# Performance work log

Hardware: AMD Instinct MI355X
Metric: run time of the kernel (lower is better)

Reference implementation:

```python
import jax, jax.numpy as jnp
import numpy as np

B, T, D, V, L = 32, 512, 512, 1024, 128
BLANK = 0
NEG = -1e30  # log-domain 'minus infinity' that is fp-safe


def setup_inputs() -> dict:
    key = jax.random.key(0)
    k1, k2, k3 = jax.random.split(key, 3)
    x = jax.random.normal(k1, (B, T, D), dtype=jnp.float32)
    W = jax.random.normal(k2, (D, V), dtype=jnp.float32) / np.sqrt(D).astype(np.float32)
    b = jnp.zeros((V,), dtype=jnp.float32)
    # CTC targets must be in [1, V) (never the blank id 0)
    target = jax.random.randint(k3, (B, L), 1, V)
    input_lengths = jnp.full((B,), T, dtype=jnp.int32)
    target_lengths = jnp.full((B,), L, dtype=jnp.int32)
    return {"x": x, "W": W, "b": b, "target": target,
            "input_lengths": input_lengths, "target_lengths": target_lengths}


def _ctc_loss(log_probs, target, input_lengths, target_lengths):
    # log_probs: [T, B, V] (time-major), target: [B, L]
    Tt, Bb, _ = log_probs.shape
    Ll = target.shape[1]
    S = 2 * Ll + 1  # extended label sequence: blank,t0,blank,t1,...,blank
    ext = jnp.full((Bb, S), BLANK, dtype=target.dtype).at[:, 1::2].set(target)  # [B,S]
    ext_m2 = jnp.pad(ext, ((0, 0), (2, 0)), constant_values=BLANK)[:, :S]
    skip = (ext != BLANK) & (ext != ext_m2) & (jnp.arange(S)[None, :] >= 2)  # [B,S]

    # gather log-probs of extended labels for every time step: [T,B,S]
    lp_ext = jnp.take_along_axis(log_probs, jnp.broadcast_to(ext[None], (Tt, Bb, S)), axis=2)

    alpha0 = jnp.full((Bb, S), NEG, log_probs.dtype)
    alpha0 = alpha0.at[:, 0].set(lp_ext[0, :, 0]).at[:, 1].set(lp_ext[0, :, 1])

    def step(alpha, lp_t):
        a1 = jnp.pad(alpha, ((0, 0), (1, 0)), constant_values=NEG)[:, :S]
        a2 = jnp.pad(alpha, ((0, 0), (2, 0)), constant_values=NEG)[:, :S]
        c = jnp.logaddexp(alpha, a1)
        c = jnp.where(skip, jnp.logaddexp(c, a2), c)
        new = c + lp_t
        return new, new

    _, alphas = jax.lax.scan(step, alpha0, lp_ext[1:])
    alphas = jnp.concatenate([alpha0[None], alphas], axis=0)  # [T,B,S]

    bi = jnp.arange(Bb)
    a_last = alphas[input_lengths - 1, bi]  # [B,S] alpha at each sample's final frame
    ll = jnp.logaddexp(a_last[bi, 2 * target_lengths - 1], a_last[bi, 2 * target_lengths])
    nll = -ll  # per-sample negative log-likelihood
    # zero_infinity=True: infinite losses are zeroed
    nll = jnp.where(jnp.isinf(nll) | (nll > 1e29), 0.0, nll)
    # reduction='mean': divide each loss by its target length, then mean
    return jnp.mean(nll / jnp.maximum(target_lengths, 1).astype(nll.dtype))


def reference(x, W, b, target, input_lengths, target_lengths):
    logits = jnp.einsum('btd,dv->btv', x, W) + b  # nn.Linear
    log_probs = jax.nn.log_softmax(logits, axis=-1)  # [B,T,V]
    return _ctc_loss(jnp.transpose(log_probs, (1, 0, 2)), target, input_lengths, target_lengths)
```

## Files before the change

### kernel.cpp

```cpp
#include <hip/hip_runtime.h>
#include <cstdint>


#define PROW 256
#define PEXT_PAD_ROWS 64
#define NPROD 6
#define NSLOT 4
#define L2E 1.4426950408889634f
#define LN2 0.6931471805599453f

typedef short v8s __attribute__((ext_vector_type(8)));
typedef float v4f __attribute__((ext_vector_type(4)));

__device__ __forceinline__ uint32_t f2bf_bits(float f) {
  uint32_t u = __float_as_uint(f);
  return (u + 0x7FFFu + ((u >> 16) & 1u)) >> 16;
}
__device__ __forceinline__ float bf2f(uint32_t h) { return __uint_as_float(h << 16); }

__global__ void k_prep(const float* __restrict__ x, uint16_t* __restrict__ xb, long long n,
                       const float* __restrict__ W, uint16_t* __restrict__ Wt, int D, int V,
                       float* __restrict__ out, int nconv) {
  if (blockIdx.x == 0 && threadIdx.x == 0) out[0] = 0.f;
  if ((int)blockIdx.x < nconv) {
    long long i = ((long long)blockIdx.x * blockDim.x + threadIdx.x) * 8;
    if (i >= n) return;
    float4 a = *(const float4*)(x + i);
    float4 b = *(const float4*)(x + i + 4);
    uint4 o;
    o.x = f2bf_bits(a.x) | (f2bf_bits(a.y) << 16);
    o.y = f2bf_bits(a.z) | (f2bf_bits(a.w) << 16);
    o.z = f2bf_bits(b.x) | (f2bf_bits(b.y) << 16);
    o.w = f2bf_bits(b.z) | (f2bf_bits(b.w) << 16);
    *(uint4*)(xb + i) = o;
  } else {
    __shared__ float tile[32][33];
    const int bid2 = blockIdx.x - nconv;
    const int n0 = (bid2 % (V / 32)) * 32, k0 = (bid2 / (V / 32)) * 32;
    const int tx = threadIdx.x & 31, ty = threadIdx.x >> 5;
    #pragma unroll
    for (int i = 0; i < 32; i += 8)
      tile[ty + i][tx] = W[(size_t)(k0 + ty + i) * V + n0 + tx];
    __syncthreads();
    #pragma unroll
    for (int i = 0; i < 32; i += 8)
      Wt[(size_t)(n0 + ty + i) * D + k0 + tx] = (uint16_t)f2bf_bits(tile[tx][ty + i]);
  }
}

__global__ __launch_bounds__(256) void k_gemm(const uint16_t* __restrict__ A,
                                              const uint16_t* __restrict__ Bt,
                                              const float* __restrict__ bias,
                                              uint16_t* __restrict__ C, int M, int N, int K) {
  __shared__ uint16_t As[2][128 * 32];
  __shared__ uint16_t Bs[2][128 * 32];
  const int tid = threadIdx.x, lane = tid & 63, wave = tid >> 6;
  int d = blockIdx.x;
  const int nwg = gridDim.x;
  if ((nwg & 7) == 0) d = (d & 7) * (nwg >> 3) + (d >> 3);
  const int ntl = N >> 7;
  const int m0 = (d / ntl) * 128, n0 = (d % ntl) * 128;
  const int wm = wave & 1, wn = wave >> 1;
  const int frow = lane & 15, kb = lane >> 4;
  const int lr = lane >> 2, kc = lane & 3;
  v4f acc[4][4] = {};

  for (int k0 = 0; k0 < K; k0 += 64) {
    __syncthreads();
    #pragma unroll
    for (int t = 0; t < 2; t++)
      #pragma unroll
      for (int i = 0; i < 2; i++) {
        const int r = (wave * 2 + i) * 16 + lr;
        const uint16_t* ga = A + (size_t)(m0 + r) * K + k0 + t * 32 + kc * 8;
        const uint16_t* gb = Bt + (size_t)(n0 + r) * K + k0 + t * 32 + kc * 8;
        __builtin_amdgcn_global_load_lds(
            (const __attribute__((address_space(1))) void*)ga,
            (__attribute__((address_space(3))) void*)(&As[t][0] + (wave * 2 + i) * 512 + lane * 8), 16, 0, 0);
        __builtin_amdgcn_global_load_lds(
            (const __attribute__((address_space(1))) void*)gb,
            (__attribute__((address_space(3))) void*)(&Bs[t][0] + (wave * 2 + i) * 512 + lane * 8), 16, 0, 0);
      }
    __syncthreads();

    #pragma unroll
    for (int t = 0; t < 2; t++) {
      v8s af[4], bf[4];
      #pragma unroll
      for (int i = 0; i < 4; i++)
        af[i] = *(const v8s*)(&As[t][0] + (wm * 64 + i * 16 + frow) * 32 + kb * 8);
      #pragma unroll
      for (int j = 0; j < 4; j++)
        bf[j] = *(const v8s*)(&Bs[t][0] + (wn * 64 + j * 16 + frow) * 32 + kb * 8);
      #pragma unroll
      for (int i = 0; i < 4; i++)
        #pragma unroll
        for (int j = 0; j < 4; j++)
          acc[i][j] = __builtin_amdgcn_mfma_f32_16x16x32_bf16(af[i], bf[j], acc[i][j], 0, 0, 0);
    }
  }

  const int crow = (lane >> 4) * 4, ccol = lane & 15;
  #pragma unroll
  for (int j = 0; j < 4; j++) {
    const int n = n0 + wn * 64 + j * 16 + ccol;
    const float bv = bias[n];
    #pragma unroll
    for (int i = 0; i < 4; i++) {
      const int mb = m0 + wm * 64 + i * 16 + crow;
      #pragma unroll
      for (int r2 = 0; r2 < 4; r2++)
        C[(size_t)(mb + r2) * N + n] = (uint16_t)f2bf_bits(acc[i][j][r2] + bv);
    }
  }
}

__global__ void k_softmax_gather(const uint16_t* __restrict__ logits, const int* __restrict__ target,
                                 const int* __restrict__ tlen, float* __restrict__ pext,
                                 int T, int V, int L) {
  const int row = blockIdx.x * 4 + (threadIdx.x >> 6);
  const int lane = threadIdx.x & 63;
  const uint16_t* lrow = logits + (size_t)row * V;

  float xs[16];
  int cnt = 0;
  float mx = -INFINITY;
  for (int base = 0; base < V; base += 256) {
    const int idx = base + lane * 4;
    uint2 u = *(const uint2*)(lrow + idx);
    float4 v;
    v.x = bf2f(u.x & 0xFFFFu); v.y = bf2f(u.x >> 16);
    v.z = bf2f(u.y & 0xFFFFu); v.w = bf2f(u.y >> 16);
    xs[cnt] = v.x; xs[cnt + 1] = v.y; xs[cnt + 2] = v.z; xs[cnt + 3] = v.w; cnt += 4;
    mx = fmaxf(mx, fmaxf(fmaxf(v.x, v.y), fmaxf(v.z, v.w)));
  }
  #pragma unroll
  for (int off = 32; off; off >>= 1) mx = fmaxf(mx, __shfl_xor(mx, off, 64));
  float sum = 0.f;
  #pragma unroll
  for (int q = 0; q < 16; q++) { if (q < cnt) sum += exp2f((xs[q] - mx) * L2E); }
  #pragma unroll
  for (int off = 32; off; off >>= 1) sum += __shfl_xor(sum, off, 64);
  const float lse2 = mx * L2E + log2f(sum);

  const int bidx = row / T;
  const int Lb = tlen[bidx];
  const int S = 2 * Lb + 1;
  float* prow = pext + (size_t)row * PROW;
  #pragma unroll
  for (int it = 0; it < PROW / 64; it++) {
    const int s = lane + it * 64;
    float p = 0.f;
    if (s < S) {
      const int lbl = (s & 1) ? target[bidx * L + ((s - 1) >> 1)] : 0;
      p = exp2f(bf2f(lrow[lbl]) * L2E - lse2);
    }
    prow[s] = p;
  }
}

__device__ __forceinline__ float wave_shr1(float x) {
  return __int_as_float(__builtin_amdgcn_update_dpp(0, __float_as_int(x), 0x138, 0xf, 0xf, true));
}
__device__ __forceinline__ float wave_max_nonneg(float x) {
  x = fmaxf(x, __int_as_float(__builtin_amdgcn_update_dpp(0, __float_as_int(x), 0x111, 0xf, 0xf, true)));
  x = fmaxf(x, __int_as_float(__builtin_amdgcn_update_dpp(0, __float_as_int(x), 0x112, 0xf, 0xf, true)));
  x = fmaxf(x, __int_as_float(__builtin_amdgcn_update_dpp(0, __float_as_int(x), 0x114, 0xf, 0xf, true)));
  x = fmaxf(x, __int_as_float(__builtin_amdgcn_update_dpp(0, __float_as_int(x), 0x118, 0xf, 0xf, true)));
  x = fmaxf(x, __int_as_float(__builtin_amdgcn_update_dpp(0, __float_as_int(x), 0x142, 0xf, 0xf, true)));
  x = fmaxf(x, __int_as_float(__builtin_amdgcn_update_dpp(0, __float_as_int(x), 0x143, 0xf, 0xf, true)));
  return __int_as_float(__builtin_amdgcn_readlane(__float_as_int(x), 63));
}

__global__ __launch_bounds__(448, 1) void k_ctc(const float* __restrict__ pext,
                                                const int* __restrict__ target,
                                                const int* __restrict__ ilen,
                                                const int* __restrict__ tlen,
                                                float* __restrict__ out, int T, int L) {
  __shared__ __attribute__((aligned(16))) float ring[NSLOT][8][PROW];
  __shared__ float abuf[257];

  const int b = blockIdx.x;
  const int tid = threadIdx.x;
  const int lane = tid & 63, wave = tid >> 6;
  const int B = gridDim.x;
  const int Tb = ilen[b];
  const int Lb = tlen[b];
  const int S = 2 * Lb + 1;
  const int* tg = target + b * L;
  const float* pb = pext + (size_t)b * T * PROW;
  const int CT = (Tb - 1) / 8 + 1;

  if (wave > 0) {
    const int p = wave - 1;
    float4 P0, P1, P2, P3, P4, P5, P6, P7;

    #define LOADCHUNK(c) {                                                  \
      const float* s_ = pb + (size_t)(1 + 8 * (c)) * PROW + (lane << 2);    \
      P0 = *(const float4*)(s_);            P1 = *(const float4*)(s_ + PROW);     \
      P2 = *(const float4*)(s_ + 2 * PROW); P3 = *(const float4*)(s_ + 3 * PROW); \
      P4 = *(const float4*)(s_ + 4 * PROW); P5 = *(const float4*)(s_ + 5 * PROW); \
      P6 = *(const float4*)(s_ + 6 * PROW); P7 = *(const float4*)(s_ + 7 * PROW); }
    #define WRITECHUNK(c) {                                                 \
      const int sl_ = (c) & (NSLOT - 1);                                    \
      *(float4*)(&ring[sl_][0][lane << 2]) = P0; *(float4*)(&ring[sl_][1][lane << 2]) = P1; \
      *(float4*)(&ring[sl_][2][lane << 2]) = P2; *(float4*)(&ring[sl_][3][lane << 2]) = P3; \
      *(float4*)(&ring[sl_][4][lane << 2]) = P4; *(float4*)(&ring[sl_][5][lane << 2]) = P5; \
      *(float4*)(&ring[sl_][6][lane << 2]) = P6; *(float4*)(&ring[sl_][7][lane << 2]) = P7; }

    if (p < CT) LOADCHUNK(p);
    if (p == 0 && 0 < CT) {
      WRITECHUNK(0);
      asm volatile("s_waitcnt lgkmcnt(0)" ::: "memory");
      if (NPROD < CT) LOADCHUNK(NPROD);
      __builtin_amdgcn_sched_barrier(0);
    }
    __builtin_amdgcn_s_barrier();

    for (int c = 0; c < CT; ++c) {
      const int cpub = c + 1;
      if (cpub < CT && (cpub % NPROD) == p) {
        WRITECHUNK(cpub);
        asm volatile("s_waitcnt lgkmcnt(0)" ::: "memory");
        const int cn = cpub + NPROD;
        if (cn < CT) LOADCHUNK(cn);
        __builtin_amdgcn_sched_barrier(0);
      }
      __builtin_amdgcn_s_barrier();
    }
    return;
  }

  const int s1 = 4 * lane + 1, s3 = 4 * lane + 3;
  float sk1 = 0.f, sk3 = 0.f;
  if (s1 >= 3 && s1 < S) sk1 = (tg[(s1 - 1) >> 1] != tg[(s1 - 3) >> 1]) ? 1.f : 0.f;
  if (s3 >= 3 && s3 < S) sk3 = (tg[(s3 - 1) >> 1] != tg[(s3 - 3) >> 1]) ? 1.f : 0.f;

  const float4 p0 = *(const float4*)(pb + (lane << 2));
  float a0 = (lane == 0) ? p0.x : 0.f;
  float a1 = (lane == 0) ? p0.y : 0.f;
  float a2 = 0.f, a3 = 0.f, a4 = 0.f;
  float log2C = 0.f;

  #define CTC_STEP(PP) {                                                \
    const float pm3 = wave_shr1(a3);                                    \
    const float a255 = __int_as_float(__builtin_amdgcn_readlane(__float_as_int(a3), 63)); \
    const float p4v = __int_as_float(__builtin_amdgcn_readlane(__float_as_int((PP).x), 0)); \
    const float n0v = (a0 + pm3) * (PP).x;                              \
    const float n1v = (a1 + a0 + sk1 * pm3) * (PP).y;                   \
    const float n2v = (a2 + a1) * (PP).z;                               \
    const float n3v = (a3 + a2 + sk3 * a1) * (PP).w;                    \
    const float n4v = (a4 + a255) * p4v;                                \
    a0 = n0v; a1 = n1v; a2 = n2v; a3 = n3v; a4 = n4v; }

  #define RENORM {                                                      \
    float m = fmaxf(fmaxf(fmaxf(a0, a1), fmaxf(a2, a3)), a4);           \
    m = wave_max_nonneg(m);                                             \
    const int e = (int)((__float_as_uint(m) >> 23) & 255u) - 127;       \
    const float scale = __uint_as_float((uint32_t)(127 - e) << 23);     \
    a0 *= scale; a1 *= scale; a2 *= scale; a3 *= scale; a4 *= scale;    \
    log2C += (float)e; }

  __builtin_amdgcn_s_barrier();

  for (int c = 0; c < CT; ++c) {
    const int slot = c & (NSLOT - 1);
    float4 P[8];
    #pragma unroll
    for (int k = 0; k < 8; ++k)
      P[k] = *(const float4*)(&ring[slot][k][lane << 2]);
    const int t0 = 1 + 8 * c;
    if (t0 + 8 <= Tb) {
      #pragma unroll
      for (int k = 0; k < 8; ++k) CTC_STEP(P[k]);
      RENORM;
    } else {
      #pragma unroll
      for (int k = 0; k < 8; ++k) { if (t0 + k < Tb) CTC_STEP(P[k]); }
      RENORM;
    }
    __builtin_amdgcn_s_barrier();
  }

  abuf[4 * lane + 0] = a0; abuf[4 * lane + 1] = a1;
  abuf[4 * lane + 2] = a2; abuf[4 * lane + 3] = a3;
  if (lane == 63) abuf[256] = a4;
  if (lane == 0) {
    const float ssum = abuf[2 * Lb - 1] + abuf[2 * Lb];
    const float ll = (log2f(ssum) + log2C) * LN2;
    float nll = -ll;
    if (!(nll < 1e29f)) nll = 0.f;
    atomicAdd(out, nll / ((float)(Lb > 0 ? Lb : 1) * (float)B));
  }
}

extern "C" void kernel_launch(void* const* d_in, const int* in_sizes, int n_in,
                              void* d_out, int out_size, void* d_ws, size_t ws_size,
                              hipStream_t stream) {
  const float* x      = (const float*)d_in[0];
  const float* W      = (const float*)d_in[1];
  const float* bias   = (const float*)d_in[2];
  const int*  target  = (const int*)d_in[3];
  const int*  ilen    = (const int*)d_in[4];
  const int*  tlen    = (const int*)d_in[5];

  const int B = in_sizes[4];
  const int V = in_sizes[2];
  const int D = in_sizes[1] / V;
  const int T = in_sizes[0] / (B * D);
  const int L = in_sizes[3] / B;
  const int M = B * T;

  char* ws = (char*)d_ws;
  const size_t xb_bytes = (size_t)M * D * 2;
  const size_t wt_bytes = (size_t)V * D * 2;
  uint16_t* xb = (uint16_t*)ws;
  uint16_t* Wt = (uint16_t*)(ws + xb_bytes);
  uint16_t* logits = (uint16_t*)(ws + xb_bytes + wt_bytes);
  const size_t log_bytes = (size_t)M * V * 2;

  const size_t pext_bytes = (size_t)(M + PEXT_PAD_ROWS) * PROW * 4;
  float* pext;
  if (pext_bytes <= xb_bytes + wt_bytes) {
    pext = (float*)ws;
  } else {
    pext = (float*)(ws + xb_bytes + wt_bytes + log_bytes);
  }

  const long long nx = (long long)M * D;
  const int nconv = (int)((nx / 8 + 255) / 256);
  const int ntrans = (V / 32) * (D / 32);
  k_prep<<<nconv + ntrans, 256, 0, stream>>>(x, xb, nx, W, Wt, D, V, (float*)d_out, nconv);
  k_gemm<<<(M / 128) * (V / 128), 256, 0, stream>>>(xb, Wt, bias, logits, M, V, D);
  k_softmax_gather<<<M / 4, 256, 0, stream>>>(logits, target, tlen, pext, T, V, L);
  k_ctc<<<B, 64 * (1 + NPROD), 0, stream>>>(pext, target, ilen, tlen, (float*)d_out, T, L);
}
```

Before: 155.2 us.

## Fuse softmax normalizer and label gather into GEMM epilogue

Removes the separate softmax/gather kernel and the bf16 logits round-trip through global memory. The GEMM epilogue stages its output tile in shared memory, accumulates per-row sums of exp(logit) via atomics into a zeroed sumrow buffer, and writes unnormalized exp values for the blank and target labels into pext. The CTC kernel subtracts the summed log2 normalizers at the end, since normalisation factors out of the alpha recursion. This relies on exp without max-subtraction, which can overflow for large logits, and adds atomics plus a scattered per-label pext write loop.

New measurement: 189.0 us. +21.8%, slower.

```diff
diff --git a/kernel.cpp b/kernel.cpp
--- a/kernel.cpp
+++ b/kernel.cpp
@@ -20,7 +20,8 @@
 
 __global__ void k_prep(const float* __restrict__ x, uint16_t* __restrict__ xb, long long n,
                        const float* __restrict__ W, uint16_t* __restrict__ Wt, int D, int V,
-                       float* __restrict__ out, int nconv) {
+                       float* __restrict__ out, float* __restrict__ sumrow, int M,
+                       int nconv, int ntrans) {
   if (blockIdx.x == 0 && threadIdx.x == 0) out[0] = 0.f;
   if ((int)blockIdx.x < nconv) {
     long long i = ((long long)blockIdx.x * blockDim.x + threadIdx.x) * 8;
@@ -33,7 +34,7 @@
     o.z = f2bf_bits(b.x) | (f2bf_bits(b.y) << 16);
     o.w = f2bf_bits(b.z) | (f2bf_bits(b.w) << 16);
     *(uint4*)(xb + i) = o;
-  } else {
+  } else if ((int)blockIdx.x < nconv + ntrans) {
     __shared__ float tile[32][33];
     const int bid2 = blockIdx.x - nconv;
     const int n0 = (bid2 % (V / 32)) * 32, k0 = (bid2 / (V / 32)) * 32;
@@ -45,15 +46,24 @@
     #pragma unroll
     for (int i = 0; i < 32; i += 8)
       Wt[(size_t)(n0 + ty + i) * D + k0 + tx] = (uint16_t)f2bf_bits(tile[tx][ty + i]);
+  } else {
+    const int bid3 = blockIdx.x - nconv - ntrans;
+    const long long i4 = ((long long)bid3 * 256 + threadIdx.x) * 4;
+    if (i4 + 3 < M) *(float4*)(sumrow + i4) = make_float4(0.f, 0.f, 0.f, 0.f);
   }
 }
 
 __global__ __launch_bounds__(256) void k_gemm(const uint16_t* __restrict__ A,
                                               const uint16_t* __restrict__ Bt,
                                               const float* __restrict__ bias,
-                                              uint16_t* __restrict__ C, int M, int N, int K) {
-  __shared__ uint16_t As[2][128 * 32];
-  __shared__ uint16_t Bs[2][128 * 32];
+                                              const int* __restrict__ target,
+                                              const int* __restrict__ tlen,
+                                              float* __restrict__ pext,
+                                              float* __restrict__ sumrow,
+                                              int M, int N, int K, int T, int L) {
+  __shared__ uint16_t SM[4 * 128 * 32];
+  #define AS(t) (SM + (t) * 4096)
+  #define BS(t) (SM + 8192 + (t) * 4096)
   const int tid = threadIdx.x, lane = tid & 63, wave = tid >> 6;
   int d = blockIdx.x;
   const int nwg = gridDim.x;
@@ -76,10 +86,10 @@
         const uint16_t* gb = Bt + (size_t)(n0 + r) * K + k0 + t * 32 + kc * 8;
         __builtin_amdgcn_global_load_lds(
             (const __attribute__((address_space(1))) void*)ga,
-            (__attribute__((address_space(3))) void*)(&As[t][0] + (wave * 2 + i) * 512 + lane * 8), 16, 0, 0);
+            (__attribute__((address_space(3))) void*)(AS(t) + (wave * 2 + i) * 512 + lane * 8), 16, 0, 0);
         __builtin_amdgcn_global_load_lds(
             (const __attribute__((address_space(1))) void*)gb,
-            (__attribute__((address_space(3))) void*)(&Bs[t][0] + (wave * 2 + i) * 512 + lane * 8), 16, 0, 0);
+            (__attribute__((address_space(3))) void*)(BS(t) + (wave * 2 + i) * 512 + lane * 8), 16, 0, 0);
       }
     __syncthreads();
 
@@ -88,10 +98,10 @@
       v8s af[4], bf[4];
       #pragma unroll
       for (int i = 0; i < 4; i++)
-        af[i] = *(const v8s*)(&As[t][0] + (wm * 64 + i * 16 + frow) * 32 + kb * 8);
+        af[i] = *(const v8s*)(AS(t) + (wm * 64 + i * 16 + frow) * 32 + kb * 8);
       #pragma unroll
       for (int j = 0; j < 4; j++)
-        bf[j] = *(const v8s*)(&Bs[t][0] + (wn * 64 + j * 16 + frow) * 32 + kb * 8);
+        bf[j] = *(const v8s*)(BS(t) + (wn * 64 + j * 16 + frow) * 32 + kb * 8);
       #pragma unroll
       for (int i = 0; i < 4; i++)
         #pragma unroll
@@ -100,62 +110,61 @@
     }
   }
 
+  __syncthreads();
   const int crow = (lane >> 4) * 4, ccol = lane & 15;
+  float rs[4][4];
+  #pragma unroll
+  for (int i = 0; i < 4; i++)
+    #pragma unroll
+    for (int r2 = 0; r2 < 4; r2++) rs[i][r2] = 0.f;
   #pragma unroll
   for (int j = 0; j < 4; j++) {
-    const int n = n0 + wn * 64 + j * 16 + ccol;
-    const float bv = bias[n];
+    const int nc = wn * 64 + j * 16 + ccol;
+    const float bv = bias[n0 + nc];
     #pragma unroll
     for (int i = 0; i < 4; i++) {
-      const int mb = m0 + wm * 64 + i * 16 + crow;
-      #pragma unroll
-      for (int r2 = 0; r2 < 4; r2++)
-        C[(size_t)(mb + r2) * N + n] = (uint16_t)f2bf_bits(acc[i][j][r2] + bv);
-    }
-  }
-}
-
-__global__ void k_softmax_gather(const uint16_t* __restrict__ logits, const int* __restrict__ target,
-                                 const int* __restrict__ tlen, float* __restrict__ pext,
-                                 int T, int V, int L) {
-  const int row = blockIdx.x * 4 + (threadIdx.x >> 6);
-  const int lane = threadIdx.x & 63;
-  const uint16_t* lrow = logits + (size_t)row * V;
-
-  float xs[16];
-  int cnt = 0;
-  float mx = -INFINITY;
-  for (int base = 0; base < V; base += 256) {
-    const int idx = base + lane * 4;
-    uint2 u = *(const uint2*)(lrow + idx);
-    float4 v;
-    v.x = bf2f(u.x & 0xFFFFu); v.y = bf2f(u.x >> 16);
-    v.z = bf2f(u.y & 0xFFFFu); v.w = bf2f(u.y >> 16);
-    xs[cnt] = v.x; xs[cnt + 1] = v.y; xs[cnt + 2] = v.z; xs[cnt + 3] = v.w; cnt += 4;
-    mx = fmaxf(mx, fmaxf(fmaxf(v.x, v.y), fmaxf(v.z, v.w)));
+      const int rr = wm * 64 + i * 16 + crow;
+      #pragma unroll
+      for (int r2 = 0; r2 < 4; r2++) {
+        const uint16_t hb = (uint16_t)f2bf_bits(acc[i][j][r2] + bv);
+        SM[(rr + r2) * 128 + nc] = hb;
+        rs[i][r2] += exp2f(bf2f(hb) * L2E);
+      }
+    }
   }
   #pragma unroll
-  for (int off = 32; off; off >>= 1) mx = fmaxf(mx, __shfl_xor(mx, off, 64));
-  float sum = 0.f;
-  #pragma unroll
-  for (int q = 0; q < 16; q++) { if (q < cnt) sum += exp2f((xs[q] - mx) * L2E); }
-  #pragma unroll
-  for (int off = 32; off; off >>= 1) sum += __shfl_xor(sum, off, 64);
-  const float lse2 = mx * L2E + log2f(sum);
-
-  const int bidx = row / T;
-  const int Lb = tlen[bidx];
-  const int S = 2 * Lb + 1;
-  float* prow = pext + (size_t)row * PROW;
-  #pragma unroll
-  for (int it = 0; it < PROW / 64; it++) {
-    const int s = lane + it * 64;
-    float p = 0.f;
-    if (s < S) {
-      const int lbl = (s & 1) ? target[bidx * L + ((s - 1) >> 1)] : 0;
-      p = exp2f(bf2f(lrow[lbl]) * L2E - lse2);
-    }
-    prow[s] = p;
+  for (int i = 0; i < 4; i++)
+    #pragma unroll
+    for (int r2 = 0; r2 < 4; r2++) {
+      float s_ = rs[i][r2];
+      s_ += __shfl_xor(s_, 1, 64); s_ += __shfl_xor(s_, 2, 64);
+      s_ += __shfl_xor(s_, 4, 64); s_ += __shfl_xor(s_, 8, 64);
+      if (ccol == 0)
+        atomicAdd(&sumrow[m0 + wm * 64 + i * 16 + crow + r2], s_);
+    }
+  __syncthreads();
+
+  const int bb = m0 / T;
+  const int Lb2 = tlen[bb];
+  {
+    const int w = tid;
+    const int j = w >> 1, rh = (w & 1) * 64;
+    const int lbl = (j < Lb2 && j < L) ? target[bb * L + j] : -1;
+    if (lbl >= n0 && lbl < n0 + 128) {
+      const int lc = lbl - n0;
+      for (int r = 0; r < 64; r++)
+        pext[(size_t)(m0 + rh + r) * PROW + 2 * j + 1] =
+            exp2f(bf2f(SM[(rh + r) * 128 + lc]) * L2E);
+    } else if (n0 == 0 && lbl < 0) {
+      for (int r = 0; r < 64; r++)
+        pext[(size_t)(m0 + rh + r) * PROW + 2 * j + 1] = 0.f;
+    }
+  }
+  if (n0 == 0) {
+    const int r = tid >> 1, h = tid & 1;
+    const float bu = exp2f(bf2f(SM[r * 128 + 0]) * L2E);
+    for (int k = h * 64; k < h * 64 + 64; k++)
+      pext[(size_t)(m0 + r) * PROW + 2 * k] = bu;
   }
 }
 
@@ -173,6 +182,7 @@
 }
 
 __global__ __launch_bounds__(448, 1) void k_ctc(const float* __restrict__ pext,
+                                                const float* __restrict__ sumrow,
                                                 const int* __restrict__ target,
                                                 const int* __restrict__ ilen,
                                                 const int* __restrict__ tlen,
@@ -285,9 +295,15 @@
   abuf[4 * lane + 0] = a0; abuf[4 * lane + 1] = a1;
   abuf[4 * lane + 2] = a2; abuf[4 * lane + 3] = a3;
   if (lane == 63) abuf[256] = a4;
+
+  float sl = 0.f;
+  for (int t = lane; t < Tb; t += 64) sl += log2f(sumrow[(size_t)b * T + t]);
+  #pragma unroll
+  for (int off = 32; off; off >>= 1) sl += __shfl_xor(sl, off, 64);
+
   if (lane == 0) {
     const float ssum = abuf[2 * Lb - 1] + abuf[2 * Lb];
-    const float ll = (log2f(ssum) + log2C) * LN2;
+    const float ll = (log2f(ssum) + log2C - sl) * LN2;
     float nll = -ll;
     if (!(nll < 1e29f)) nll = 0.f;
     atomicAdd(out, nll / ((float)(Lb > 0 ? Lb : 1) * (float)B));
@@ -314,24 +330,20 @@
   char* ws = (char*)d_ws;
   const size_t xb_bytes = (size_t)M * D * 2;
   const size_t wt_bytes = (size_t)V * D * 2;
+  const size_t pext_bytes = (size_t)(M + PEXT_PAD_ROWS) * PROW * 4;
   uint16_t* xb = (uint16_t*)ws;
   uint16_t* Wt = (uint16_t*)(ws + xb_bytes);
-  uint16_t* logits = (uint16_t*)(ws + xb_bytes + wt_bytes);
-  const size_t log_bytes = (size_t)M * V * 2;
-
-  const size_t pext_bytes = (size_t)(M + PEXT_PAD_ROWS) * PROW * 4;
-  float* pext;
-  if (pext_bytes <= xb_bytes + wt_bytes) {
-    pext = (float*)ws;
-  } else {
-    pext = (float*)(ws + xb_bytes + wt_bytes + log_bytes);
-  }
+  float* pext   = (float*)(ws + xb_bytes + wt_bytes);
+  float* sumrow = (float*)(ws + xb_bytes + wt_bytes + pext_bytes);
 
   const long long nx = (long long)M * D;
   const int nconv = (int)((nx / 8 + 255) / 256);
   const int ntrans = (V / 32) * (D / 32);
-  k_prep<<<nconv + ntrans, 256, 0, stream>>>(x, xb, nx, W, Wt, D, V, (float*)d_out, nconv);
-  k_gemm<<<(M / 128) * (V / 128), 256, 0, stream>>>(xb, Wt, bias, logits, M, V, D);
-  k_softmax_gather<<<M / 4, 256, 0, stream>>>(logits, target, tlen, pext, T, V, L);
-  k_ctc<<<B, 64 * (1 + NPROD), 0, stream>>>(pext, target, ilen, tlen, (float*)d_out, T, L);
-}
+  const int nzero = (M + 256 * 4 - 1) / (256 * 4);
+  k_prep<<<nconv + ntrans + nzero, 256, 0, stream>>>(x, xb, nx, W, Wt, D, V,
+                                                     (float*)d_out, sumrow, M, nconv, ntrans);
+  k_gemm<<<(M / 128) * (V / 128), 256, 0, stream>>>(xb, Wt, bias, target, tlen,
+                                                    pext, sumrow, M, V, D, T, L);
+  k_ctc<<<B, 64 * (1 + NPROD), 0, stream>>>(pext, sumrow, target, ilen, tlen,
+                                            (float*)d_out, T, L);
+}
```
